# Kernel tuning notes

Hardware: AMD Instinct MI355X
Metric: run time of the kernel (lower is better)

## Reference

```python
import jax, jax.numpy as jnp
import numpy as np

N_NODES = 10000
N_EDGES = 320000


def _segment_softmax(scores, seg, num_segments):
    # scores: [E, H], segment-wise stable softmax keyed by seg (edge_index[0])
    m = jax.ops.segment_max(scores, seg, num_segments=num_segments)
    e = jnp.exp(scores - m[seg])
    z = jax.ops.segment_sum(e, seg, num_segments=num_segments)
    return e / z[seg]


def _gat_layer(x, W, a, row, col, n_nodes, heads, out_dim):
    # x: [N, F_in], W: [F_in, heads*out_dim], a: [heads, 2*out_dim]
    h = (x @ W).reshape(n_nodes, heads, out_dim)          # [N, H, F]
    a_l, a_r = a[:, :out_dim], a[:, out_dim:]             # [H, F] each
    # attention score per edge/head without materializing [E, H, 2F]
    s = (h[row] * a_l).sum(-1) + (h[col] * a_r).sum(-1)   # [E, H]
    alpha = _segment_softmax(s, row, n_nodes)             # [E, H]
    msg = alpha[..., None] * h[row]                       # [E, H, F]
    return jax.ops.segment_sum(msg, col, num_segments=n_nodes)  # [N, H, F]


def setup_inputs() -> dict:
    key = jax.random.key(0)
    ks = jax.random.split(key, 6)
    F, H, C = 128, 4, 22
    x = jax.random.normal(ks[0], (N_NODES, F), dtype=jnp.float32)
    edge_index = jax.random.randint(ks[1], (2, N_EDGES), 0, N_NODES, dtype=jnp.int64)
    W1 = jax.random.normal(ks[2], (F, F * H), dtype=jnp.float32) * 0.05
    a1 = jax.random.normal(ks[3], (H, 2 * F), dtype=jnp.float32) * 0.05
    W2 = jax.random.normal(ks[4], (F, C), dtype=jnp.float32) * 0.05
    a2 = jax.random.normal(ks[5], (1, 2 * C), dtype=jnp.float32) * 0.05
    return {"x": x, "edge_index": edge_index, "W1": W1, "a1": a1, "W2": W2, "a2": a2}


def reference(x, edge_index, W1, a1, W2, a2):
    row, col = edge_index[0], edge_index[1]
    h1 = _gat_layer(x, W1, a1, row, col, N_NODES, heads=4, out_dim=128)  # [N, 4, 128]
    h1 = jax.nn.elu(h1).mean(axis=1)                                      # combine heads -> [N, 128]
    h2 = _gat_layer(h1, W2, a2, row, col, N_NODES, heads=1, out_dim=22)   # [N, 1, 22]
    return h2[:, 0, :]                                                    # [N, 22]
```

## Files before the change

### kernel.cpp

```cpp
#include <hip/hip_runtime.h>

#define NN 10000
#define NE 320000
#define EPP 5000
#define NPART 64

typedef short short8 __attribute__((ext_vector_type(8)));
typedef float f32x4 __attribute__((ext_vector_type(4)));

__device__ __forceinline__ unsigned short f2bf(float f) {
    unsigned u = __float_as_uint(f);
    return (unsigned short)((u + 0x7FFFu + ((u >> 16) & 1u)) >> 16);
}
__device__ __forceinline__ float bflo(unsigned v) { return __uint_as_float(v << 16); }
__device__ __forceinline__ float bfhi(unsigned v) { return __uint_as_float(v & 0xffff0000u); }
__device__ __forceinline__ float bf1(unsigned short v) { return __uint_as_float(((unsigned)v) << 16); }

__device__ __forceinline__ int eread(const void* p, int is64, int i) {
    if (is64) return (int)((const long long*)p)[i];
    return ((const int*)p)[i];
}

__global__ __launch_bounds__(256) void k_prep0(const void* __restrict__ ei,
                                               const float* __restrict__ W1, const float* __restrict__ a1,
                                               unsigned short* __restrict__ W1t, float* __restrict__ wrf,
                                               int* __restrict__ flag) {
    const int b = blockIdx.x, t = threadIdx.x;
    if (b < 256) {
        const int g = b * 256 + t;
        const int h = g >> 14, j = (g >> 7) & 127, k = g & 127;
        W1t[g] = f2bf(W1[(size_t)k * 512 + h * 128 + j]);
    } else if (b < 258) {
        const int g = (b - 256) * 256 + t;
        const int h = g >> 7, k = g & 127;
        const float* wrow = W1 + (size_t)k * 512 + h * 128;
        const float* av = a1 + h * 256 + 128;
        float s = 0.f;
        for (int d = 0; d < 128; d++) s += wrow[d] * av[d];
        wrf[h * 128 + k] = s;
    } else {
        if (t == 0) {
            const unsigned* idx = (const unsigned*)ei;
            int all0 = 1;
            for (int j = 1; j < 257; j += 2)
                if (idx[j] != 0u) { all0 = 0; break; }
            *flag = all0;
        }
    }
}

__global__ __launch_bounds__(256) void k_pre(const float* __restrict__ x, const float* __restrict__ wrf,
                                             unsigned short* __restrict__ xb, float* __restrict__ ehr1,
                                             const void* __restrict__ ei, const int* __restrict__ flag,
                                             unsigned short* __restrict__ degp_c,
                                             unsigned short* __restrict__ degp_r,
                                             unsigned* __restrict__ packed_c,
                                             unsigned* __restrict__ packed_r) {
    __shared__ int sh[NN];
    const int b = blockIdx.x, t = threadIdx.x;
    if (b < 2500) {
        float* ls = (float*)sh;
        const int lane = t & 63, w = t >> 6;
        ls[t] = wrf[t];
        ls[t + 256] = wrf[t + 256];
        __syncthreads();
        const int i = b * 4 + w;
        const float x0 = x[(size_t)i * 128 + lane];
        const float x1 = x[(size_t)i * 128 + 64 + lane];
        xb[(size_t)i * 128 + lane]      = f2bf(x0);
        xb[(size_t)i * 128 + 64 + lane] = f2bf(x1);
        float v[4];
#pragma unroll
        for (int h = 0; h < 4; h++)
            v[h] = x0 * ls[h * 128 + lane] + x1 * ls[h * 128 + 64 + lane];
#pragma unroll
        for (int off = 1; off < 64; off <<= 1) {
#pragma unroll
            for (int j = 0; j < 4; j++) v[j] += __shfl_xor(v[j], off);
        }
        if (lane == 0)
            *(float4*)&ehr1[i * 4] = make_float4(__expf(v[0]), __expf(v[1]), __expf(v[2]), __expf(v[3]));
    } else {
        const int is64 = *flag;
        const int isC = (b < 2500 + NPART);
        const int p = isC ? (b - 2500) : (b - 2500 - NPART);
        const int ebase = p * EPP;
        for (int q = t; q < NN; q += 256) sh[q] = 0;
        __syncthreads();
        if (isC) {
            for (int q = t; q < EPP; q += 256) {
                const int e = ebase + q;
                const int c = eread(ei, is64, NE + e);
                const unsigned rk = (unsigned)atomicAdd(&sh[c], 1);
                packed_c[e] = ((unsigned)c << 13) | rk;
            }
            __syncthreads();
            for (int q = t; q < NN; q += 256) degp_c[p * NN + q] = (unsigned short)sh[q];
        } else {
            for (int q = t; q < EPP; q += 256) {
                const int e = ebase + q;
                const int r = eread(ei, is64, e);
                const unsigned rk = (unsigned)atomicAdd(&sh[r], 1);
                packed_r[e] = ((unsigned)r << 13) | rk;
            }
            __syncthreads();
            for (int q = t; q < NN; q += 256) degp_r[p * NN + q] = (unsigned short)sh[q];
        }
    }
}

__global__ __launch_bounds__(256) void k_psum(const unsigned short* __restrict__ degp_c,
                                              const unsigned short* __restrict__ degp_r,
                                              unsigned short* __restrict__ pfx_c,
                                              unsigned short* __restrict__ pfx_r,
                                              int* __restrict__ deg_c, int* __restrict__ deg_r) {
    const int g = blockIdx.x * 256 + threadIdx.x;
    if (g >= 2 * NN) return;
    const int arr = g / NN, node = g % NN;
    const unsigned short* degp = arr ? degp_r : degp_c;
    unsigned short* pfx = arr ? pfx_r : pfx_c;
    int* tot = arr ? deg_r : deg_c;
    int sum = 0;
#pragma unroll
    for (int p = 0; p < NPART; p++) {
        pfx[p * NN + node] = (unsigned short)sum;
        sum += (int)degp[p * NN + node];
    }
    tot[node] = sum;
}

__device__ void scan_one_1k(const int* __restrict__ deg, int* __restrict__ start, int* ssum) {
    const int t = threadIdx.x;
    int loc[10];
    const int base = t * 10;
    int sum = 0;
#pragma unroll
    for (int j = 0; j < 10; j++) {
        int i = base + j;
        int v = (i < NN) ? deg[i] : 0;
        loc[j] = sum;
        sum += v;
    }
    const int lane = t & 63, w = t >> 6;
    int xi = sum;
#pragma unroll
    for (int off = 1; off < 64; off <<= 1) {
        int y = __shfl_up(xi, off);
        if (lane >= off) xi += y;
    }
    __syncthreads();
    if (lane == 63) ssum[w] = xi;
    __syncthreads();
    int woff = 0;
#pragma unroll
    for (int k = 0; k < 16; k++)
        if (k < w) woff += ssum[k];
    const int excl = woff + xi - sum;
#pragma unroll
    for (int j = 0; j < 10; j++) {
        int i = base + j;
        if (i < NN) start[i] = excl + loc[j];
    }
}

__global__ __launch_bounds__(1024) void k_scan2(const int* __restrict__ deg_c, const int* __restrict__ deg_r,
                                                int* __restrict__ start_c, int* __restrict__ start_r) {
    __shared__ int ssum[16];
    scan_one_1k(deg_c, start_c, ssum);
    __syncthreads();
    scan_one_1k(deg_r, start_r, ssum);
}

__global__ __launch_bounds__(256) void k_build(const unsigned* __restrict__ packed_c,
                                               const unsigned* __restrict__ packed_r,
                                               const unsigned short* __restrict__ pfx_c,
                                               const unsigned short* __restrict__ pfx_r,
                                               const int* __restrict__ start_c, const int* __restrict__ start_r,
                                               int* __restrict__ csrA, int* __restrict__ csrB) {
    const int e = blockIdx.x * 256 + threadIdx.x;
    if (e >= NE) return;
    const int part = e / EPP;
    const unsigned pc = packed_c[e], pr = packed_r[e];
    const int c = (int)(pc >> 13), rkc = (int)(pc & 8191u);
    const int r = (int)(pr >> 13), rkr = (int)(pr & 8191u);
    csrA[start_c[c] + (int)pfx_c[part * NN + c] + rkc] = r;
    csrB[start_r[r] + (int)pfx_r[part * NN + r] + rkr] = c;
}

__global__ __launch_bounds__(256) void k_z1(const int* __restrict__ start_r, const int* __restrict__ deg_r,
                                            const int* __restrict__ csrB,
                                            const float* __restrict__ ehr1, float* __restrict__ rz1) {
    const int t = threadIdx.x, lane = t & 63, w = t >> 6;
    const int half = lane >> 5, l32 = lane & 31;
    const int i = blockIdx.x * 8 + w * 2 + half;
    const int s0 = start_r[i], d = deg_r[i];
    float zx = 0.f, zy = 0.f, zz = 0.f, zw = 0.f;
    for (int p = s0 + l32; p < s0 + d; p += 32) {
        const int c = csrB[p];
        const float4 v = *(const float4*)&ehr1[c * 4];
        zx += v.x; zy += v.y; zz += v.z; zw += v.w;
    }
#pragma unroll
    for (int off = 1; off < 32; off <<= 1) {
        zx += __shfl_xor(zx, off); zy += __shfl_xor(zy, off);
        zz += __shfl_xor(zz, off); zw += __shfl_xor(zw, off);
    }
    if (l32 == 0)
        *(float4*)&rz1[i * 4] = make_float4(1.f / zx, 1.f / zy, 1.f / zz, 1.f / zw);
}

__global__ __launch_bounds__(256) void k_agg1(const unsigned short* __restrict__ xb,
                                              const float* __restrict__ ehr1, const float* __restrict__ rz1,
                                              const int* __restrict__ start_c, const int* __restrict__ deg_c,
                                              const int* __restrict__ csrA,
                                              unsigned short* __restrict__ xaggb) {
    const int t = threadIdx.x, lane = t & 63, w = t >> 6;
    const int i = blockIdx.x * 4 + w;
    const float4 er4 = *(const float4*)&ehr1[i * 4];
    const int s0 = start_c[i], dg = deg_c[i];
    float acc[8];
#pragma unroll
    for (int j = 0; j < 8; j++) acc[j] = 0.f;
    int p = s0;
    const int e8 = s0 + (dg & ~7);
    for (; p < e8; p += 8) {
        int rr[8]; unsigned vv[8]; float4 zz[8];
#pragma unroll
        for (int q = 0; q < 8; q++) rr[q] = csrA[p + q];
#pragma unroll
        for (int q = 0; q < 8; q++) vv[q] = *(const unsigned*)&xb[(size_t)rr[q] * 128 + lane * 2];
#pragma unroll
        for (int q = 0; q < 8; q++) zz[q] = *(const float4*)&rz1[rr[q] * 4];
#pragma unroll
        for (int q = 0; q < 8; q++) {
            const float xa = bflo(vv[q]), xbv = bfhi(vv[q]);
            acc[0] += zz[q].x * xa; acc[1] += zz[q].x * xbv;
            acc[2] += zz[q].y * xa; acc[3] += zz[q].y * xbv;
            acc[4] += zz[q].z * xa; acc[5] += zz[q].z * xbv;
            acc[6] += zz[q].w * xa; acc[7] += zz[q].w * xbv;
        }
    }
    for (; p < s0 + dg; ++p) {
        const int r = csrA[p];
        const unsigned v = *(const unsigned*)&xb[(size_t)r * 128 + lane * 2];
        const float4 z = *(const float4*)&rz1[r * 4];
        const float xa = bflo(v), xbv = bfhi(v);
        acc[0] += z.x * xa; acc[1] += z.x * xbv;
        acc[2] += z.y * xa; acc[3] += z.y * xbv;
        acc[4] += z.z * xa; acc[5] += z.z * xbv;
        acc[6] += z.w * xa; acc[7] += z.w * xbv;
    }
    const float ef[4] = {er4.x, er4.y, er4.z, er4.w};
    unsigned short* op = xaggb + (size_t)i * 512 + lane * 2;
#pragma unroll
    for (int h = 0; h < 4; h++) {
        ushort2 st;
        st.x = f2bf(acc[h * 2] * ef[h]);
        st.y = f2bf(acc[h * 2 + 1] * ef[h]);
        *(ushort2*)(op + h * 128) = st;
    }
}

__global__ __launch_bounds__(256) void k_gemmF(const unsigned short* __restrict__ xaggb,
                                               const unsigned short* __restrict__ W1t,
                                               float* __restrict__ h1m) {
    const int t = threadIdx.x, lane = t & 63, w = t >> 6;
    const int n0 = blockIdx.x * 32;
    const int r16 = lane & 15, grp = lane >> 4;
    const int jbase = w * 32;
    f32x4 hm[2][2];
#pragma unroll
    for (int m = 0; m < 2; m++)
#pragma unroll
        for (int n = 0; n < 2; n++) hm[m][n] = (f32x4)0.f;

#pragma unroll
    for (int h = 0; h < 4; h++) {
        f32x4 acc[2][2];
#pragma unroll
        for (int m = 0; m < 2; m++)
#pragma unroll
            for (int n = 0; n < 2; n++) acc[m][n] = (f32x4)0.f;
#pragma unroll
        for (int kk = 0; kk < 128; kk += 32) {
            const int k0 = kk + grp * 8;
            short8 a0 = *(const short8*)&xaggb[((size_t)(n0 + r16) * 4 + h) * 128 + k0];
            short8 a1 = *(const short8*)&xaggb[((size_t)(n0 + 16 + r16) * 4 + h) * 128 + k0];
            short8 b0 = *(const short8*)&W1t[(size_t)h * 16384 + (jbase + r16) * 128 + k0];
            short8 b1 = *(const short8*)&W1t[(size_t)h * 16384 + (jbase + 16 + r16) * 128 + k0];
            acc[0][0] = __builtin_amdgcn_mfma_f32_16x16x32_bf16(a0, b0, acc[0][0], 0, 0, 0);
            acc[1][0] = __builtin_amdgcn_mfma_f32_16x16x32_bf16(a1, b0, acc[1][0], 0, 0, 0);
            acc[0][1] = __builtin_amdgcn_mfma_f32_16x16x32_bf16(a0, b1, acc[0][1], 0, 0, 0);
            acc[1][1] = __builtin_amdgcn_mfma_f32_16x16x32_bf16(a1, b1, acc[1][1], 0, 0, 0);
        }
#pragma unroll
        for (int m = 0; m < 2; m++)
#pragma unroll
            for (int n = 0; n < 2; n++)
#pragma unroll
                for (int r = 0; r < 4; r++) {
                    const float v = acc[m][n][r];
                    hm[m][n][r] += (v > 0.f) ? v : (__expf(v) - 1.f);
                }
    }
#pragma unroll
    for (int m = 0; m < 2; m++)
#pragma unroll
        for (int n = 0; n < 2; n++)
#pragma unroll
            for (int r = 0; r < 4; r++) {
                const int node = n0 + m * 16 + grp * 4 + r;
                const int col = jbase + n * 16 + r16;
                h1m[(size_t)node * 128 + col] = 0.25f * hm[m][n][r];
            }
}

__global__ __launch_bounds__(256) void k_gemm2(const float* __restrict__ h1m, const float* __restrict__ W2,
                                               const float* __restrict__ a2,
                                               float* __restrict__ h2, float* __restrict__ ehr2) {
    __shared__ float sh[4][128];
    const int t = threadIdx.x, lane = t & 63, w = t >> 6;
    const int i = blockIdx.x * 4 + w;
    sh[w][lane]      = h1m[(size_t)i * 128 + lane];
    sh[w][lane + 64] = h1m[(size_t)i * 128 + 64 + lane];
    __syncthreads();
    const int seg = lane >> 5, c = lane & 31;
    float part = 0.f;
    if (c < 22) {
        const int kb = seg * 64;
        for (int k = kb; k < kb + 64; k++)
            part += sh[w][k] * W2[k * 22 + c];
    }
    part += __shfl_xor(part, 32);
    const float acc = part;
    if (lane < 22) h2[(size_t)i * 22 + lane] = acc;
    float pr = (lane < 22) ? acc * a2[22 + lane] : 0.f;
#pragma unroll
    for (int off = 1; off < 64; off <<= 1)
        pr += __shfl_xor(pr, off);
    if (lane == 0) ehr2[i] = __expf(pr);
}

__global__ __launch_bounds__(256) void k_z2s(const int* __restrict__ start_r, const int* __restrict__ deg_r,
                                             const int* __restrict__ csrB,
                                             const float* __restrict__ ehr2, const float* __restrict__ h2,
                                             unsigned short* __restrict__ h2s) {
    const int t = threadIdx.x, lane = t & 63, w = t >> 6;
    const int half = lane >> 5, l32 = lane & 31;
    const int i = blockIdx.x * 8 + w * 2 + half;
    const int s0 = start_r[i], d = deg_r[i];
    float z = 0.f;
    for (int p = s0 + l32; p < s0 + d; p += 32)
        z += ehr2[csrB[p]];
#pragma unroll
    for (int off = 1; off < 32; off <<= 1)
        z += __shfl_xor(z, off);
    const float rz = 1.f / z;
    if (l32 < 22)
        h2s[(size_t)i * 32 + l32] = f2bf(h2[(size_t)i * 22 + l32] * rz);
}

__global__ __launch_bounds__(256) void k_agg2(const unsigned short* __restrict__ h2s,
                                              const float* __restrict__ ehr2,
                                              const int* __restrict__ start_c, const int* __restrict__ deg_c,
                                              const int* __restrict__ csrA,
                                              float* __restrict__ out) {
    const int t = threadIdx.x, lane = t & 63, w = t >> 6;
    const int half = lane >> 5, c32 = lane & 31;
    const int i = blockIdx.x * 8 + w * 2 + half;
    const int s0 = start_c[i], dg = deg_c[i];
    const float e2 = ehr2[i];
    const int c = (c32 < 22) ? c32 : 0;
    float acc = 0.f;
    int p = s0;
    const int e8 = s0 + (dg & ~7);
    for (; p < e8; p += 8) {
        int rr[8];
#pragma unroll
        for (int q = 0; q < 8; q++) rr[q] = csrA[p + q];
        float vv[8];
#pragma unroll
        for (int q = 0; q < 8; q++) vv[q] = bf1(h2s[(size_t)rr[q] * 32 + c]);
#pragma unroll
        for (int q = 0; q < 8; q++) acc += vv[q];
    }
    for (; p < s0 + dg; ++p) {
        const int r = csrA[p];
        acc += bf1(h2s[(size_t)r * 32 + c]);
    }
    if (c32 < 22) out[(size_t)i * 22 + c32] = acc * e2;
}

extern "C" void kernel_launch(void* const* d_in, const int* in_sizes, int n_in,
                              void* d_out, int out_size, void* d_ws, size_t ws_size,
                              hipStream_t stream) {
    const float* x  = (const float*)d_in[0];
    const void*  ei = d_in[1];
    const float* W1 = (const float*)d_in[2];
    const float* a1 = (const float*)d_in[3];
    const float* W2 = (const float*)d_in[4];
    const float* a2 = (const float*)d_in[5];
    float* out = (float*)d_out;

    float* ws = (float*)d_ws;
    unsigned short* xaggb = (unsigned short*)ws;
    float* h1m  = ws + 2600000;
    float* h2   = ws + 3890000;
    float* ehr1 = ws + 4110000;
    float* rz1  = ws + 4150000;
    float* ehr2 = ws + 4190000;
    unsigned short* h2s = (unsigned short*)(ws + 4200000);
    int* deg_c   = (int*)(ws + 4360000);
    int* deg_r   = (int*)(ws + 4370000);
    int* start_c = (int*)(ws + 4380000);
    int* start_r = (int*)(ws + 4390000);
    int* csrA    = (int*)(ws + 4400000);
    int* csrB    = (int*)(ws + 4720000);
    int* flag    = (int*)(ws + 5040000);
    float* wrf   = ws + 5040064;
    unsigned short* W1t = (unsigned short*)(ws + 5041000);
    unsigned short* xb  = (unsigned short*)(ws + 5074000);
    unsigned* packed_c = (unsigned*)(ws + 5714000);
    unsigned* packed_r = (unsigned*)(ws + 6034000);
    unsigned short* degp_c = (unsigned short*)(ws + 6354000);
    unsigned short* degp_r = (unsigned short*)(ws + 6674000);
    unsigned short* pfx_c  = (unsigned short*)(ws + 6994000);
    unsigned short* pfx_r  = (unsigned short*)(ws + 7314000);

    k_prep0<<<259, 256, 0, stream>>>(ei, W1, a1, W1t, wrf, flag);
    k_pre<<<2500 + 2 * NPART, 256, 0, stream>>>(x, wrf, xb, ehr1, ei, flag,
                                                degp_c, degp_r, packed_c, packed_r);
    k_psum<<<79, 256, 0, stream>>>(degp_c, degp_r, pfx_c, pfx_r, deg_c, deg_r);
    k_scan2<<<1, 1024, 0, stream>>>(deg_c, deg_r, start_c, start_r);
    k_build<<<1250, 256, 0, stream>>>(packed_c, packed_r, pfx_c, pfx_r,
                                      start_c, start_r, csrA, csrB);
    k_z1<<<1250, 256, 0, stream>>>(start_r, deg_r, csrB, ehr1, rz1);
    k_agg1<<<2500, 256, 0, stream>>>(xb, ehr1, rz1, start_c, deg_c, csrA, xaggb);
    k_gemmF<<<313, 256, 0, stream>>>(xaggb, W1t, h1m);
    k_gemm2<<<2500, 256, 0, stream>>>(h1m, W2, a2, h2, ehr2);
    k_z2s<<<1250, 256, 0, stream>>>(start_r, deg_r, csrB, ehr2, h2, h2s);
    k_agg2<<<1250, 256, 0, stream>>>(h2s, ehr2, start_c, deg_c, csrA, out);
}
```

Measured before the change: 112.3 us.

## Fuse layer-1 aggregation with head GEMM via swizzled LDS tile

```diff
diff --git a/kernel.cpp b/kernel.cpp
--- a/kernel.cpp
+++ b/kernel.cpp
@@ -209,110 +209,93 @@
         *(float4*)&rz1[i * 4] = make_float4(1.f / zx, 1.f / zy, 1.f / zz, 1.f / zw);
 }
 
-__global__ __launch_bounds__(256) void k_agg1(const unsigned short* __restrict__ xb,
-                                              const float* __restrict__ ehr1, const float* __restrict__ rz1,
-                                              const int* __restrict__ start_c, const int* __restrict__ deg_c,
-                                              const int* __restrict__ csrA,
-                                              unsigned short* __restrict__ xaggb) {
-    const int t = threadIdx.x, lane = t & 63, w = t >> 6;
-    const int i = blockIdx.x * 4 + w;
-    const float4 er4 = *(const float4*)&ehr1[i * 4];
-    const int s0 = start_c[i], dg = deg_c[i];
-    float acc[8];
-#pragma unroll
-    for (int j = 0; j < 8; j++) acc[j] = 0.f;
-    int p = s0;
-    const int e8 = s0 + (dg & ~7);
-    for (; p < e8; p += 8) {
-        int rr[8]; unsigned vv[8]; float4 zz[8];
-#pragma unroll
-        for (int q = 0; q < 8; q++) rr[q] = csrA[p + q];
-#pragma unroll
-        for (int q = 0; q < 8; q++) vv[q] = *(const unsigned*)&xb[(size_t)rr[q] * 128 + lane * 2];
-#pragma unroll
-        for (int q = 0; q < 8; q++) zz[q] = *(const float4*)&rz1[rr[q] * 4];
-#pragma unroll
-        for (int q = 0; q < 8; q++) {
-            const float xa = bflo(vv[q]), xbv = bfhi(vv[q]);
-            acc[0] += zz[q].x * xa; acc[1] += zz[q].x * xbv;
-            acc[2] += zz[q].y * xa; acc[3] += zz[q].y * xbv;
-            acc[4] += zz[q].z * xa; acc[5] += zz[q].z * xbv;
-            acc[6] += zz[q].w * xa; acc[7] += zz[q].w * xbv;
-        }
-    }
-    for (; p < s0 + dg; ++p) {
-        const int r = csrA[p];
-        const unsigned v = *(const unsigned*)&xb[(size_t)r * 128 + lane * 2];
-        const float4 z = *(const float4*)&rz1[r * 4];
-        const float xa = bflo(v), xbv = bfhi(v);
-        acc[0] += z.x * xa; acc[1] += z.x * xbv;
-        acc[2] += z.y * xa; acc[3] += z.y * xbv;
-        acc[4] += z.z * xa; acc[5] += z.z * xbv;
-        acc[6] += z.w * xa; acc[7] += z.w * xbv;
-    }
-    const float ef[4] = {er4.x, er4.y, er4.z, er4.w};
-    unsigned short* op = xaggb + (size_t)i * 512 + lane * 2;
-#pragma unroll
-    for (int h = 0; h < 4; h++) {
-        ushort2 st;
-        st.x = f2bf(acc[h * 2] * ef[h]);
-        st.y = f2bf(acc[h * 2 + 1] * ef[h]);
-        *(ushort2*)(op + h * 128) = st;
-    }
-}
-
-__global__ __launch_bounds__(256) void k_gemmF(const unsigned short* __restrict__ xaggb,
+__global__ __launch_bounds__(1024) void k_aggF(const unsigned short* __restrict__ xb,
+                                               const float* __restrict__ ehr1, const float* __restrict__ rz1,
+                                               const int* __restrict__ start_c, const int* __restrict__ deg_c,
+                                               const int* __restrict__ csrA,
                                                const unsigned short* __restrict__ W1t,
                                                float* __restrict__ h1m) {
+    __shared__ unsigned short lx[16 * 512];
     const int t = threadIdx.x, lane = t & 63, w = t >> 6;
-    const int n0 = blockIdx.x * 32;
-    const int r16 = lane & 15, grp = lane >> 4;
-    const int jbase = w * 32;
-    f32x4 hm[2][2];
-#pragma unroll
-    for (int m = 0; m < 2; m++)
-#pragma unroll
-        for (int n = 0; n < 2; n++) hm[m][n] = (f32x4)0.f;
-
-#pragma unroll
-    for (int h = 0; h < 4; h++) {
-        f32x4 acc[2][2];
-#pragma unroll
-        for (int m = 0; m < 2; m++)
-#pragma unroll
-            for (int n = 0; n < 2; n++) acc[m][n] = (f32x4)0.f;
-#pragma unroll
-        for (int kk = 0; kk < 128; kk += 32) {
-            const int k0 = kk + grp * 8;
-            short8 a0 = *(const short8*)&xaggb[((size_t)(n0 + r16) * 4 + h) * 128 + k0];
-            short8 a1 = *(const short8*)&xaggb[((size_t)(n0 + 16 + r16) * 4 + h) * 128 + k0];
-            short8 b0 = *(const short8*)&W1t[(size_t)h * 16384 + (jbase + r16) * 128 + k0];
-            short8 b1 = *(const short8*)&W1t[(size_t)h * 16384 + (jbase + 16 + r16) * 128 + k0];
-            acc[0][0] = __builtin_amdgcn_mfma_f32_16x16x32_bf16(a0, b0, acc[0][0], 0, 0, 0);
-            acc[1][0] = __builtin_amdgcn_mfma_f32_16x16x32_bf16(a1, b0, acc[1][0], 0, 0, 0);
-            acc[0][1] = __builtin_amdgcn_mfma_f32_16x16x32_bf16(a0, b1, acc[0][1], 0, 0, 0);
-            acc[1][1] = __builtin_amdgcn_mfma_f32_16x16x32_bf16(a1, b1, acc[1][1], 0, 0, 0);
-        }
-#pragma unroll
-        for (int m = 0; m < 2; m++)
-#pragma unroll
-            for (int n = 0; n < 2; n++)
-#pragma unroll
-                for (int r = 0; r < 4; r++) {
-                    const float v = acc[m][n][r];
-                    hm[m][n][r] += (v > 0.f) ? v : (__expf(v) - 1.f);
-                }
-    }
-#pragma unroll
-    for (int m = 0; m < 2; m++)
-#pragma unroll
-        for (int n = 0; n < 2; n++)
+    const int n0 = blockIdx.x * 16;
+
+    {
+        const int i = n0 + w;
+        const float4 er4 = *(const float4*)&ehr1[i * 4];
+        const int s0 = start_c[i], dg = deg_c[i];
+        float acc[8];
+#pragma unroll
+        for (int j = 0; j < 8; j++) acc[j] = 0.f;
+        int p = s0;
+        const int e8 = s0 + (dg & ~7);
+        for (; p < e8; p += 8) {
+            int rr[8]; unsigned vv[8]; float4 zz[8];
+#pragma unroll
+            for (int q = 0; q < 8; q++) rr[q] = csrA[p + q];
+#pragma unroll
+            for (int q = 0; q < 8; q++) vv[q] = *(const unsigned*)&xb[(size_t)rr[q] * 128 + lane * 2];
+#pragma unroll
+            for (int q = 0; q < 8; q++) zz[q] = *(const float4*)&rz1[rr[q] * 4];
+#pragma unroll
+            for (int q = 0; q < 8; q++) {
+                const float xa = bflo(vv[q]), xbv = bfhi(vv[q]);
+                acc[0] += zz[q].x * xa; acc[1] += zz[q].x * xbv;
+                acc[2] += zz[q].y * xa; acc[3] += zz[q].y * xbv;
+                acc[4] += zz[q].z * xa; acc[5] += zz[q].z * xbv;
+                acc[6] += zz[q].w * xa; acc[7] += zz[q].w * xbv;
+            }
+        }
+        for (; p < s0 + dg; ++p) {
+            const int r = csrA[p];
+            const unsigned v = *(const unsigned*)&xb[(size_t)r * 128 + lane * 2];
+            const float4 z = *(const float4*)&rz1[r * 4];
+            const float xa = bflo(v), xbv = bfhi(v);
+            acc[0] += z.x * xa; acc[1] += z.x * xbv;
+            acc[2] += z.y * xa; acc[3] += z.y * xbv;
+            acc[4] += z.z * xa; acc[5] += z.z * xbv;
+            acc[6] += z.w * xa; acc[7] += z.w * xbv;
+        }
+        const float ef[4] = {er4.x, er4.y, er4.z, er4.w};
+        const int fin = (lane & 3) * 2;
+#pragma unroll
+        for (int h = 0; h < 4; h++) {
+            const int f = h * 16 + (lane >> 2);
+            const int sc = ((f ^ (w & 7)) << 3) + fin;
+            ushort2 st;
+            st.x = f2bf(acc[h * 2] * ef[h]);
+            st.y = f2bf(acc[h * 2 + 1] * ef[h]);
+            *(ushort2*)&lx[w * 512 + sc] = st;
+        }
+    }
+    __syncthreads();
+
+    if (w < 8) {
+        const int j = w;
+        const int r16 = lane & 15, grp = lane >> 4;
+        f32x4 hm = (f32x4)0.f;
+#pragma unroll
+        for (int h = 0; h < 4; h++) {
+            f32x4 acc = (f32x4)0.f;
+#pragma unroll
+            for (int kk = 0; kk < 128; kk += 32) {
+                const int f = h * 16 + (kk >> 3) + grp;
+                const int sc = (f ^ (r16 & 7)) << 3;
+                short8 a = *(const short8*)&lx[r16 * 512 + sc];
+                short8 bfr = *(const short8*)&W1t[(size_t)h * 16384 + (j * 16 + r16) * 128 + kk + grp * 8];
+                acc = __builtin_amdgcn_mfma_f32_16x16x32_bf16(a, bfr, acc, 0, 0, 0);
+            }
 #pragma unroll
             for (int r = 0; r < 4; r++) {
-                const int node = n0 + m * 16 + grp * 4 + r;
-                const int col = jbase + n * 16 + r16;
-                h1m[(size_t)node * 128 + col] = 0.25f * hm[m][n][r];
+                const float v = acc[r];
+                hm[r] += (v > 0.f) ? v : (__expf(v) - 1.f);
             }
+        }
+#pragma unroll
+        for (int r = 0; r < 4; r++) {
+            const int node = n0 + grp * 4 + r;
+            h1m[(size_t)node * 128 + j * 16 + r16] = 0.25f * hm[r];
+        }
+    }
 }
 
 __global__ __launch_bounds__(256) void k_gemm2(const float* __restrict__ h1m, const float* __restrict__ W2,
@@ -403,29 +386,28 @@
     float* out = (float*)d_out;
 
     float* ws = (float*)d_ws;
-    unsigned short* xaggb = (unsigned short*)ws;
-    float* h1m  = ws + 2600000;
-    float* h2   = ws + 3890000;
-    float* ehr1 = ws + 4110000;
-    float* rz1  = ws + 4150000;
-    float* ehr2 = ws + 4190000;
-    unsigned short* h2s = (unsigned short*)(ws + 4200000);
-    int* deg_c   = (int*)(ws + 4360000);
-    int* deg_r   = (int*)(ws + 4370000);
-    int* start_c = (int*)(ws + 4380000);
-    int* start_r = (int*)(ws + 4390000);
-    int* csrA    = (int*)(ws + 4400000);
-    int* csrB    = (int*)(ws + 4720000);
-    int* flag    = (int*)(ws + 5040000);
-    float* wrf   = ws + 5040064;
-    unsigned short* W1t = (unsigned short*)(ws + 5041000);
-    unsigned short* xb  = (unsigned short*)(ws + 5074000);
-    unsigned* packed_c = (unsigned*)(ws + 5714000);
-    unsigned* packed_r = (unsigned*)(ws + 6034000);
-    unsigned short* degp_c = (unsigned short*)(ws + 6354000);
-    unsigned short* degp_r = (unsigned short*)(ws + 6674000);
-    unsigned short* pfx_c  = (unsigned short*)(ws + 6994000);
-    unsigned short* pfx_r  = (unsigned short*)(ws + 7314000);
+    float* h1m  = ws;
+    float* h2   = ws + 1280000;
+    float* ehr1 = ws + 1500000;
+    float* rz1  = ws + 1540000;
+    float* ehr2 = ws + 1580000;
+    unsigned short* h2s = (unsigned short*)(ws + 1590000);
+    int* deg_c   = (int*)(ws + 1750000);
+    int* deg_r   = (int*)(ws + 1760000);
+    int* start_c = (int*)(ws + 1770000);
+    int* start_r = (int*)(ws + 1780000);
+    int* csrA    = (int*)(ws + 1790000);
+    int* csrB    = (int*)(ws + 2110000);
+    int* flag    = (int*)(ws + 2430000);
+    float* wrf   = ws + 2430064;
+    unsigned short* W1t = (unsigned short*)(ws + 2431000);
+    unsigned short* xb  = (unsigned short*)(ws + 2464000);
+    unsigned* packed_c = (unsigned*)(ws + 3104000);
+    unsigned* packed_r = (unsigned*)(ws + 3424000);
+    unsigned short* degp_c = (unsigned short*)(ws + 3744000);
+    unsigned short* degp_r = (unsigned short*)(ws + 4064000);
+    unsigned short* pfx_c  = (unsigned short*)(ws + 4384000);
+    unsigned short* pfx_r  = (unsigned short*)(ws + 4704000);
 
     k_prep0<<<259, 256, 0, stream>>>(ei, W1, a1, W1t, wrf, flag);
     k_pre<<<2500 + 2 * NPART, 256, 0, stream>>>(x, wrf, xb, ehr1, ei, flag,
@@ -435,8 +417,7 @@
     k_build<<<1250, 256, 0, stream>>>(packed_c, packed_r, pfx_c, pfx_r,
                                       start_c, start_r, csrA, csrB);
     k_z1<<<1250, 256, 0, stream>>>(start_r, deg_r, csrB, ehr1, rz1);
-    k_agg1<<<2500, 256, 0, stream>>>(xb, ehr1, rz1, start_c, deg_c, csrA, xaggb);
-    k_gemmF<<<313, 256, 0, stream>>>(xaggb, W1t, h1m);
+    k_aggF<<<625, 1024, 0, stream>>>(xb, ehr1, rz1, start_c, deg_c, csrA, W1t, h1m);
     k_gemm2<<<2500, 256, 0, stream>>>(h1m, W2, a2, h2, ehr2);
     k_z2s<<<1250, 256, 0, stream>>>(start_r, deg_r, csrB, ehr2, h2, h2s);
     k_agg2<<<1250, 256, 0, stream>>>(h2s, ehr2, start_c, deg_c, csrA, out);
```

Measured after the change: 110.2 us. About the same (-1.8%).
